# Performance work log

Hardware: AMD Instinct MI355X
Metric: run time of the kernel (lower is better)

## Reference

```python
import jax, jax.numpy as jnp
import numpy as np

B, T, C, NH = 8, 512, 512, 8
HD = C // NH

def _layernorm(x, g, b, eps=1e-5):
    mu = jnp.mean(x, axis=-1, keepdims=True)
    var = jnp.var(x, axis=-1, keepdims=True)
    return (x - mu) * jax.lax.rsqrt(var + eps) * g + b

def setup_inputs() -> dict:
    key = jax.random.key(0)
    ks = jax.random.split(key, 5)
    return {
        "x": jax.random.normal(ks[0], (B, T, C), jnp.float32),
        "w_attn": jax.random.normal(ks[1], (3 * C, C), jnp.float32) * (1.0 / np.sqrt(C)),
        "b_attn": jnp.zeros((3 * C,), jnp.float32),
        "w_proj": jax.random.normal(ks[2], (C, C), jnp.float32) * (1.0 / np.sqrt(C)),
        "b_proj": jnp.zeros((C,), jnp.float32),
        "q_gamma": jnp.ones((C,), jnp.float32),
        "q_beta": jnp.zeros((C,), jnp.float32),
        "k_gamma": jnp.ones((C,), jnp.float32),
        "k_beta": jnp.zeros((C,), jnp.float32),
        "rel_emb": jax.random.normal(ks[3], (T, C), jnp.float32) * 0.02,
    }

def reference(x, w_attn, b_attn, w_proj, b_proj, q_gamma, q_beta, k_gamma, k_beta, rel_emb):
    b, t, c = x.shape
    # QKV projection (torch Linear: x @ W.T + b)
    qkv = x @ w_attn.T + b_attn                       # [B,T,3C]
    q, k, v = jnp.split(qkv, 3, axis=-1)
    # per-stream LayerNorm over full embedding dim (q_ln/k_ln = LayerNorm(n_embd))
    q = _layernorm(q, q_gamma, q_beta)
    k = _layernorm(k, k_gamma, k_beta)
    # split heads -> [B,NH,T,HD]
    q = q.reshape(b, t, NH, HD).transpose(0, 2, 1, 3)
    k = k.reshape(b, t, NH, HD).transpose(0, 2, 1, 3)
    v = v.reshape(b, t, NH, HD).transpose(0, 2, 1, 3)
    # relative-position bias: gather rel_emb[|i-j|] -> [T,T,NH,HD]
    idx = jnp.abs(jnp.arange(t)[None, :] - jnp.arange(t)[:, None])  # [T,T] int
    rel = rel_emb[idx].reshape(t, t, NH, HD)
    rel_bias = jnp.einsum("bhqd,qkhd->bhqk", q, rel)  # [B,NH,T,T]
    scale = 1.0 / np.sqrt(HD)
    scores = (jnp.einsum("bhqd,bhkd->bhqk", q, k) + rel_bias) * scale
    causal = jnp.tril(jnp.ones((t, t), bool))
    scores = jnp.where(causal[None, None], scores, jnp.finfo(scores.dtype).min)
    att = jax.nn.softmax(scores, axis=-1)
    y = jnp.einsum("bhqk,bhkd->bhqd", att, v)         # [B,NH,T,HD]
    y = y.transpose(0, 2, 1, 3).reshape(b, t, c)
    return y @ w_proj.T + b_proj
```

## Files before the change

kernel.cpp:

```cpp
#include <hip/hip_runtime.h>
#include <hip/hip_bf16.h>
#include <cstddef>

#define BB 8
#define TT 512
#define CC 512
#define NHH 8
#define HDD 64

typedef __attribute__((ext_vector_type(8))) short short8;
typedef __attribute__((ext_vector_type(4))) float f32x4;

__device__ __forceinline__ unsigned short f2bf(float f) {
    unsigned u = __float_as_uint(f);
    u += 0x7FFFu + ((u >> 16) & 1u);
    return (unsigned short)(u >> 16);
}
__device__ __forceinline__ float bf2f(unsigned short h) {
    return __uint_as_float(((unsigned)h) << 16);
}

__global__ __launch_bounds__(256) void cvt_all_k(
    const float* __restrict__ x, const float* __restrict__ wa,
    const float* __restrict__ wp, const float* __restrict__ rel,
    unsigned short* __restrict__ Xb, unsigned short* __restrict__ Wqb,
    unsigned short* __restrict__ Wpb, unsigned short* __restrict__ Relb)
{
    const int bidx = blockIdx.x;
    const float* in;
    unsigned short* out;
    int base;
    if (bidx < 2048)      { in = x;   out = Xb;   base = bidx; }
    else if (bidx < 2816) { in = wa;  out = Wqb;  base = bidx - 2048; }
    else if (bidx < 3072) { in = wp;  out = Wpb;  base = bidx - 2816; }
    else                  { in = rel; out = Relb; base = bidx - 3072; }
    const int i = base * 1024 + threadIdx.x * 4;
    const float4 v = *(const float4*)(in + i);
    unsigned short tmp[4] = {f2bf(v.x), f2bf(v.y), f2bf(v.z), f2bf(v.w)};
    *(uint2*)(out + i) = *(const uint2*)tmp;
}

__global__ __launch_bounds__(256, 2) void gemm_qkv_mfma(
    const unsigned short* __restrict__ Xb, const unsigned short* __restrict__ Wb,
    const float* __restrict__ bias, unsigned short* __restrict__ qkbuf,
    unsigned short* __restrict__ VT)
{
    __shared__ __align__(16) unsigned short lds[128 * 136];

    const int tid = threadIdx.x;
    const int w = tid >> 6, lane = tid & 63;
    const int c = lane & 15, quad = lane >> 4;
    const int wm = w >> 1, wn = w & 1;
    const int bm = blockIdx.y * 128, bn = blockIdx.x * 128;

    const unsigned short* pp[8];
#pragma unroll
    for (int l = 0; l < 8; ++l) {
        const int ci = w * 8 + l;
        if (ci < 16) {
            const int m16 = ci >> 1, kk = ci & 1;
            pp[l] = Xb + (size_t)(bm + m16 * 16 + c) * 512 + kk * 32 + quad * 8;
        } else {
            const int cb = ci - 16, n16 = cb >> 1, kk = cb & 1;
            pp[l] = Wb + (size_t)(bn + n16 * 16 + c) * 512 + kk * 32 + quad * 8;
        }
    }

    f32x4 acc[4][4];
#pragma unroll
    for (int i = 0; i < 4; ++i)
#pragma unroll
        for (int j = 0; j < 4; ++j) acc[i][j] = (f32x4){0.f, 0.f, 0.f, 0.f};

    short8 pre[8];
#pragma unroll
    for (int l = 0; l < 8; ++l) pre[l] = *(const short8*)pp[l];

    for (int k0 = 0; k0 < 512; k0 += 64) {
        __syncthreads();
#pragma unroll
        for (int l = 0; l < 8; ++l)
            *(short8*)&lds[(w * 8 + l) * 512 + lane * 8] = pre[l];
        __syncthreads();
        if (k0 + 64 < 512) {
#pragma unroll
            for (int l = 0; l < 8; ++l)
                pre[l] = *(const short8*)(pp[l] + k0 + 64);
        }
#pragma unroll
        for (int kk = 0; kk < 2; ++kk) {
            short8 af[4], bfr[4];
#pragma unroll
            for (int i = 0; i < 4; ++i)
                af[i] = *(const short8*)&lds[((wm * 4 + i) * 2 + kk) * 512 + lane * 8];
#pragma unroll
            for (int j = 0; j < 4; ++j)
                bfr[j] = *(const short8*)&lds[(16 + (wn * 4 + j) * 2 + kk) * 512 + lane * 8];
#pragma unroll
            for (int i = 0; i < 4; ++i)
#pragma unroll
                for (int j = 0; j < 4; ++j)
                    acc[i][j] = __builtin_amdgcn_mfma_f32_16x16x32_bf16(
                        af[i], bfr[j], acc[i][j], 0, 0, 0);
        }
    }

    float bj[4];
#pragma unroll
    for (int j = 0; j < 4; ++j) bj[j] = bias[bn + wn * 64 + j * 16 + c];

    if (bn < 1024) {
#pragma unroll
        for (int i = 0; i < 4; ++i)
#pragma unroll
            for (int j = 0; j < 4; ++j) {
                const int n = bn + wn * 64 + j * 16 + c;
#pragma unroll
                for (int r = 0; r < 4; ++r) {
                    const int m = bm + wm * 64 + i * 16 + quad * 4 + r;
                    qkbuf[(size_t)m * 1024 + n] = f2bf(acc[i][j][r] + bj[j]);
                }
            }
    } else {
        __syncthreads();
#pragma unroll
        for (int i = 0; i < 4; ++i)
#pragma unroll
            for (int j = 0; j < 4; ++j) {
                const int col = wn * 64 + j * 16 + c;
                const int row0 = wm * 64 + i * 16 + quad * 4;
                unsigned short t4[4];
#pragma unroll
                for (int r = 0; r < 4; ++r) t4[r] = f2bf(acc[i][j][r] + bj[j]);
                *(uint2*)&lds[col * 136 + row0] = *(const uint2*)t4;
            }
        __syncthreads();
        const int bi = bm >> 9, tb = bm & 511;
        const int hd0 = bn - 1024;
#pragma unroll
        for (int l = 0; l < 8; ++l) {
            const int idx = l * 256 + tid;
            const int col = idx >> 4, grp = idx & 15;
            const short8 v = *(const short8*)&lds[col * 136 + grp * 8];
            const int hd = hd0 + col, h = hd >> 6, d = hd & 63;
            *(short8*)(VT + ((size_t)(bi * NHH + h) * HDD + d) * TT + tb + grp * 8) = v;
        }
    }
}

__global__ __launch_bounds__(256) void ln_k(
    const unsigned short* __restrict__ qkbuf,
    const float* __restrict__ qg, const float* __restrict__ qb,
    const float* __restrict__ kg, const float* __restrict__ kb,
    unsigned short* __restrict__ Qh, unsigned short* __restrict__ Kh)
{
    const int wv = threadIdx.x >> 6, lane = threadIdx.x & 63;
    const int row = blockIdx.x * 4 + wv;
    const int bi = row >> 9, t = row & 511;
    const unsigned short* base = qkbuf + (size_t)row * 1024;

#pragma unroll
    for (int s = 0; s < 2; ++s) {
        const short8 v8 = *(const short8*)(base + s * 512 + lane * 8);
        float vf[8];
#pragma unroll
        for (int i = 0; i < 8; ++i) vf[i] = bf2f(((const unsigned short*)&v8)[i]);
        float sum = 0.f, sq = 0.f;
#pragma unroll
        for (int i = 0; i < 8; ++i) { sum += vf[i]; sq += vf[i] * vf[i]; }
#pragma unroll
        for (int off = 1; off < 64; off <<= 1) {
            sum += __shfl_xor(sum, off);
            sq += __shfl_xor(sq, off);
        }
        const float mu = sum * (1.f / 512.f);
        const float var = sq * (1.f / 512.f) - mu * mu;
        const float rsg = rsqrtf(var + 1e-5f);
        const float* gam = (s ? kg : qg) + lane * 8;
        const float* bet = (s ? kb : qb) + lane * 8;
        const float4 g0 = *(const float4*)gam, g1 = *(const float4*)(gam + 4);
        const float4 b0 = *(const float4*)bet, b1 = *(const float4*)(bet + 4);
        const float gv[8] = {g0.x, g0.y, g0.z, g0.w, g1.x, g1.y, g1.z, g1.w};
        const float bv[8] = {b0.x, b0.y, b0.z, b0.w, b1.x, b1.y, b1.z, b1.w};
        unsigned short o8[8];
#pragma unroll
        for (int i = 0; i < 8; ++i)
            o8[i] = f2bf((vf[i] - mu) * rsg * gv[i] + bv[i]);
        unsigned short* outp = s ? Kh : Qh;
        *(short8*)(outp + ((size_t)(bi * NHH + (lane >> 3)) * TT + t) * HDD
                   + (lane & 7) * 8) = *(const short8*)o8;
    }
}

#define RD_BODY(nr_)                                                            \
    {                                                                           \
        const short8 br0 = *(const short8*)&Rels[((nr_) * 2 + 0) * 512 + lane * 8]; \
        const short8 br1 = *(const short8*)&Rels[((nr_) * 2 + 1) * 512 + lane * 8]; \
        f32x4 a2 = (f32x4){0.f, 0.f, 0.f, 0.f};                                 \
        a2 = __builtin_amdgcn_mfma_f32_16x16x32_bf16(aq0, br0, a2, 0, 0, 0);    \
        a2 = __builtin_amdgcn_mfma_f32_16x16x32_bf16(aq1, br1, a2, 0, 0, 0);    \
        const int colw = (mbase + (nr_) * 16 + c) & 127;                        \
        _Pragma("unroll")                                                       \
        for (int r = 0; r < 4; ++r)                                             \
            RDs[w][(quad * 4 + r) * 132 + colw] = f2bf(a2[r]);                  \
    }

__global__ __launch_bounds__(256, 2) void attn_k(
    const unsigned short* __restrict__ Qh, const unsigned short* __restrict__ Kh,
    const unsigned short* __restrict__ VT, const unsigned short* __restrict__ Relb,
    unsigned short* __restrict__ Yb)
{
    __shared__ __align__(16) unsigned short Qs[8 * 512];
    __shared__ __align__(16) unsigned short Ks[8 * 512];
    __shared__ __align__(16) unsigned short Vs[8 * 512];
    __shared__ __align__(16) unsigned short Rels[16 * 512];
    __shared__ __align__(16) unsigned short Ps[4][16 * 72];
    __shared__ __align__(16) unsigned short RDs[4][16 * 132];

    const int tid = threadIdx.x;
    const int w = tid >> 6;
    const int lane = tid & 63;
    const int c = lane & 15;
    const int quad = lane >> 4;

    const int bid = blockIdx.x;
    const int bit0 = bid & 1, bit8 = (bid >> 8) & 1;
    const int s_ = bit0 ^ bit8;
    const int q0 = (bid >> 1) & 7;
    const int qt = s_ ? 7 - q0 : q0;
    const int h = (bid >> 4) & 7;
    const int b = ((bid >> 7) & 1) | (bit8 << 1) | (bit0 << 2);
    const int i0 = qt * 64;

    const unsigned short* Qbase = Qh + (size_t)(b * NHH + h) * TT * HDD;
    const unsigned short* Kbase = Kh + (size_t)(b * NHH + h) * TT * HDD;
    const unsigned short* Vbase = VT + (size_t)(b * NHH + h) * HDD * TT;
    const unsigned short* Rbase = Relb + h * HDD;

#pragma unroll
    for (int kk = 0; kk < 2; ++kk) {
        const unsigned short* gp =
            Qbase + (size_t)(i0 + w * 16 + c) * HDD + kk * 32 + quad * 8;
        *(short8*)&Qs[(w * 2 + kk) * 512 + lane * 8] = *(const short8*)gp;
    }

    f32x4 oacc[4];
    float m_i[4], l_i[4];
#pragma unroll
    for (int r = 0; r < 4; ++r) { m_i[r] = -1e30f; l_i[r] = 0.f; }
#pragma unroll
    for (int nd = 0; nd < 4; ++nd) oacc[nd] = (f32x4){0.f, 0.f, 0.f, 0.f};

    short8 aq0, aq1;

    for (int jt = 0; jt <= qt; ++jt) {
        const int j0 = jt * 64;
#pragma unroll
        for (int kk = 0; kk < 2; ++kk) {
            const unsigned short* gp =
                Kbase + (size_t)(j0 + w * 16 + c) * HDD + kk * 32 + quad * 8;
            *(short8*)&Ks[(w * 2 + kk) * 512 + lane * 8] = *(const short8*)gp;
        }
#pragma unroll
        for (int js = 0; js < 2; ++js) {
            const unsigned short* gp =
                Vbase + (size_t)(w * 16 + c) * TT + j0 + js * 32 + quad * 8;
            *(short8*)&Vs[(w * 2 + js) * 512 + lane * 8] = *(const short8*)gp;
        }
        const int mbase = i0 - j0 - 63;
        if (jt == 0) {
#pragma unroll
            for (int sb = 0; sb < 2; ++sb) {
#pragma unroll
                for (int kk = 0; kk < 2; ++kk) {
                    const int n16 = w * 2 + sb;
                    int mrow = mbase + n16 * 16 + c;
                    mrow = mrow < 0 ? 0 : (mrow > 511 ? 511 : mrow);
                    *(short8*)&Rels[(n16 * 2 + kk) * 512 + lane * 8] =
                        *(const short8*)(Rbase + (size_t)mrow * CC + kk * 32 + quad * 8);
                }
            }
        } else {
#pragma unroll
            for (int kk = 0; kk < 2; ++kk) {
                int mrow = mbase + w * 16 + c;
                mrow = mrow < 0 ? 0 : (mrow > 511 ? 511 : mrow);
                *(short8*)&Rels[(w * 2 + kk) * 512 + lane * 8] =
                    *(const short8*)(Rbase + (size_t)mrow * CC + kk * 32 + quad * 8);
            }
        }
        __syncthreads();

        if (jt == 0) {
            aq0 = *(const short8*)&Qs[(w * 2 + 0) * 512 + lane * 8];
            aq1 = *(const short8*)&Qs[(w * 2 + 1) * 512 + lane * 8];
        }

        f32x4 sAcc[4];
#pragma unroll
        for (int ns = 0; ns < 4; ++ns) {
            const short8 bk0 = *(const short8*)&Ks[(ns * 2 + 0) * 512 + lane * 8];
            const short8 bk1 = *(const short8*)&Ks[(ns * 2 + 1) * 512 + lane * 8];
            f32x4 a2 = (f32x4){0.f, 0.f, 0.f, 0.f};
            a2 = __builtin_amdgcn_mfma_f32_16x16x32_bf16(aq0, bk0, a2, 0, 0, 0);
            a2 = __builtin_amdgcn_mfma_f32_16x16x32_bf16(aq1, bk1, a2, 0, 0, 0);
            sAcc[ns] = a2;
        }
        if (jt == 0) {
#pragma unroll
            for (int nr = 0; nr < 8; ++nr) RD_BODY(nr)
        } else {
#pragma unroll
            for (int nr = 0; nr < 4; ++nr) RD_BODY(nr)
        }

        const int dbase = i0 - j0;
        float sc[4][4];
#pragma unroll
        for (int ns = 0; ns < 4; ++ns) {
#pragma unroll
            for (int r = 0; r < 4; ++r) {
                const int r16 = quad * 4 + r;
                const int jc = ns * 16 + c;
                const int dp = (dbase + w * 16 + r16 - jc) & 127;
                const float rdv = bf2f(RDs[w][r16 * 132 + dp]);
                const float v = (sAcc[ns][r] + rdv) * 0.125f;
                sc[ns][r] = (j0 + jc > i0 + w * 16 + r16) ? -1e30f : v;
            }
        }
        float alpha[4];
#pragma unroll
        for (int r = 0; r < 4; ++r) {
            float m = fmaxf(fmaxf(sc[0][r], sc[1][r]), fmaxf(sc[2][r], sc[3][r]));
#pragma unroll
            for (int off = 1; off < 16; off <<= 1) m = fmaxf(m, __shfl_xor(m, off));
            const float mn = fmaxf(m_i[r], m);
            alpha[r] = __expf(m_i[r] - mn);
            m_i[r] = mn;
        }
        float rs[4] = {0.f, 0.f, 0.f, 0.f};
#pragma unroll
        for (int ns = 0; ns < 4; ++ns) {
#pragma unroll
            for (int r = 0; r < 4; ++r) {
                const float p = __expf(sc[ns][r] - m_i[r]);
                rs[r] += p;
                Ps[w][(quad * 4 + r) * 72 + ns * 16 + c] = f2bf(p);
            }
        }
#pragma unroll
        for (int r = 0; r < 4; ++r) {
#pragma unroll
            for (int off = 1; off < 16; off <<= 1) rs[r] += __shfl_xor(rs[r], off);
            l_i[r] = l_i[r] * alpha[r] + rs[r];
        }
#pragma unroll
        for (int nd = 0; nd < 4; ++nd)
#pragma unroll
            for (int r = 0; r < 4; ++r) oacc[nd][r] *= alpha[r];

        const short8 ap0 = *(const short8*)&Ps[w][c * 72 + 0 * 32 + quad * 8];
        const short8 ap1 = *(const short8*)&Ps[w][c * 72 + 1 * 32 + quad * 8];
#pragma unroll
        for (int nd = 0; nd < 4; ++nd) {
            const short8 bv0 = *(const short8*)&Vs[(nd * 2 + 0) * 512 + lane * 8];
            const short8 bv1 = *(const short8*)&Vs[(nd * 2 + 1) * 512 + lane * 8];
            oacc[nd] = __builtin_amdgcn_mfma_f32_16x16x32_bf16(ap0, bv0, oacc[nd], 0, 0, 0);
            oacc[nd] = __builtin_amdgcn_mfma_f32_16x16x32_bf16(ap1, bv1, oacc[nd], 0, 0, 0);
        }
        __syncthreads();
    }

#pragma unroll
    for (int r = 0; r < 4; ++r) {
        const float inv = 1.f / l_i[r];
        const int trow = i0 + w * 16 + quad * 4 + r;
        unsigned short* yb = Yb + ((size_t)b * TT + trow) * CC + h * HDD;
#pragma unroll
        for (int nd = 0; nd < 4; ++nd)
            yb[nd * 16 + c] = f2bf(oacc[nd][r] * inv);
    }
}

__global__ __launch_bounds__(256, 2) void gemm_proj_mfma(
    const unsigned short* __restrict__ Yb, const unsigned short* __restrict__ Wp,
    const float* __restrict__ bias, float* __restrict__ out)
{
    __shared__ __align__(16) unsigned short lds[24 * 512];

    const int tid = threadIdx.x;
    const int w = tid >> 6, lane = tid & 63;
    const int c = lane & 15, quad = lane >> 4;
    const int wm = w >> 1, wn = w & 1;
    const int bm = blockIdx.y * 64, bn = blockIdx.x * 128;

    const unsigned short* pp[6];
#pragma unroll
    for (int l = 0; l < 6; ++l) {
        const int ci = w * 6 + l;
        if (ci < 8) {
            const int m16 = ci >> 1, kk = ci & 1;
            pp[l] = Yb + (size_t)(bm + m16 * 16 + c) * 512 + kk * 32 + quad * 8;
        } else {
            const int cb = ci - 8, n16 = cb >> 1, kk = cb & 1;
            pp[l] = Wp + (size_t)(bn + n16 * 16 + c) * 512 + kk * 32 + quad * 8;
        }
    }

    f32x4 acc[2][4];
#pragma unroll
    for (int i = 0; i < 2; ++i)
#pragma unroll
        for (int j = 0; j < 4; ++j) acc[i][j] = (f32x4){0.f, 0.f, 0.f, 0.f};

    short8 pre[6];
#pragma unroll
    for (int l = 0; l < 6; ++l) pre[l] = *(const short8*)pp[l];

    for (int k0 = 0; k0 < 512; k0 += 64) {
        __syncthreads();
#pragma unroll
        for (int l = 0; l < 6; ++l)
            *(short8*)&lds[(w * 6 + l) * 512 + lane * 8] = pre[l];
        __syncthreads();
        if (k0 + 64 < 512) {
#pragma unroll
            for (int l = 0; l < 6; ++l)
                pre[l] = *(const short8*)(pp[l] + k0 + 64);
        }
#pragma unroll
        for (int kk = 0; kk < 2; ++kk) {
            short8 af[2], bfr[4];
#pragma unroll
            for (int i = 0; i < 2; ++i)
                af[i] = *(const short8*)&lds[((wm * 2 + i) * 2 + kk) * 512 + lane * 8];
#pragma unroll
            for (int j = 0; j < 4; ++j)
                bfr[j] = *(const short8*)&lds[(8 + (wn * 4 + j) * 2 + kk) * 512 + lane * 8];
#pragma unroll
            for (int i = 0; i < 2; ++i)
#pragma unroll
                for (int j = 0; j < 4; ++j)
                    acc[i][j] = __builtin_amdgcn_mfma_f32_16x16x32_bf16(
                        af[i], bfr[j], acc[i][j], 0, 0, 0);
        }
    }

#pragma unroll
    for (int j = 0; j < 4; ++j) {
        const int n = bn + wn * 64 + j * 16 + c;
        const float bj = bias[n];
#pragma unroll
        for (int i = 0; i < 2; ++i)
#pragma unroll
            for (int r = 0; r < 4; ++r) {
                const int m = bm + wm * 32 + i * 16 + quad * 4 + r;
                out[(size_t)m * 512 + n] = acc[i][j][r] + bj;
            }
    }
}

extern "C" void kernel_launch(void* const* d_in, const int* in_sizes, int n_in,
                              void* d_out, int out_size, void* d_ws, size_t ws_size,
                              hipStream_t stream)
{
    const float* x      = (const float*)d_in[0];
    const float* w_attn = (const float*)d_in[1];
    const float* b_attn = (const float*)d_in[2];
    const float* w_proj = (const float*)d_in[3];
    const float* b_proj = (const float*)d_in[4];
    const float* q_g    = (const float*)d_in[5];
    const float* q_b    = (const float*)d_in[6];
    const float* k_g    = (const float*)d_in[7];
    const float* k_b    = (const float*)d_in[8];
    const float* rel    = (const float*)d_in[9];
    float* out = (float*)d_out;

    unsigned short* qkbuf = (unsigned short*)d_ws;
    unsigned short* Qh   = qkbuf + (size_t)4096 * 1024;
    unsigned short* Kh   = Qh + (size_t)4096 * 512;
    unsigned short* VT   = Kh + (size_t)4096 * 512;
    unsigned short* Relb = VT + (size_t)4096 * 512;
    unsigned short* Xb   = Relb + (size_t)512 * 512;
    unsigned short* Wqb  = Xb + (size_t)4096 * 512;
    unsigned short* Wpb  = Wqb + (size_t)1536 * 512;
    unsigned short* Yb   = qkbuf;

    cvt_all_k<<<3328, 256, 0, stream>>>(x, w_attn, w_proj, rel, Xb, Wqb, Wpb, Relb);
    gemm_qkv_mfma<<<dim3(12, 32), 256, 0, stream>>>(Xb, Wqb, b_attn, qkbuf, VT);
    ln_k<<<1024, 256, 0, stream>>>(qkbuf, q_g, q_b, k_g, k_b, Qh, Kh);
    attn_k<<<512, 256, 0, stream>>>(Qh, Kh, VT, Relb, Yb);
    gemm_proj_mfma<<<dim3(4, 64), 256, 0, stream>>>(Yb, Wpb, b_proj, out);
}
```

Baseline: 141.6 us.

## Load attention MFMA operands directly from global memory, dropping shared staging

The attention kernel no longer stages Q, K, V and relative-embedding tiles through shared memory. Each wave loads its MFMA fragments straight from global memory into registers, which removes the per-iteration block barriers and the LDS round trips. The first-tile extra rel-bias blocks are computed once before the loop. In exchange, each wave redundantly fetches the full K/V tiles (four times the global/L2 traffic per block) and uses more registers, which may lower occupancy.

```diff
diff --git a/kernel.cpp b/kernel.cpp
--- a/kernel.cpp
+++ b/kernel.cpp
@@ -192,14 +192,17 @@
     }
 }
 
-#define RD_BODY(nr_)                                                            \
+#define RD_DIRECT(nr_, mb_)                                                     \
     {                                                                           \
-        const short8 br0 = *(const short8*)&Rels[((nr_) * 2 + 0) * 512 + lane * 8]; \
-        const short8 br1 = *(const short8*)&Rels[((nr_) * 2 + 1) * 512 + lane * 8]; \
+        int mrow = (mb_) + (nr_) * 16 + c;                                      \
+        mrow = mrow < 0 ? 0 : (mrow > 511 ? 511 : mrow);                        \
+        const unsigned short* gp = Rbase + (size_t)mrow * CC + quad * 8;        \
+        const short8 br0 = *(const short8*)gp;                                  \
+        const short8 br1 = *(const short8*)(gp + 32);                           \
         f32x4 a2 = (f32x4){0.f, 0.f, 0.f, 0.f};                                 \
         a2 = __builtin_amdgcn_mfma_f32_16x16x32_bf16(aq0, br0, a2, 0, 0, 0);    \
         a2 = __builtin_amdgcn_mfma_f32_16x16x32_bf16(aq1, br1, a2, 0, 0, 0);    \
-        const int colw = (mbase + (nr_) * 16 + c) & 127;                        \
+        const int colw = ((mb_) + (nr_) * 16 + c) & 127;                        \
         _Pragma("unroll")                                                       \
         for (int r = 0; r < 4; ++r)                                             \
             RDs[w][(quad * 4 + r) * 132 + colw] = f2bf(a2[r]);                  \
@@ -210,10 +213,6 @@
     const unsigned short* __restrict__ VT, const unsigned short* __restrict__ Relb,
     unsigned short* __restrict__ Yb)
 {
-    __shared__ __align__(16) unsigned short Qs[8 * 512];
-    __shared__ __align__(16) unsigned short Ks[8 * 512];
-    __shared__ __align__(16) unsigned short Vs[8 * 512];
-    __shared__ __align__(16) unsigned short Rels[16 * 512];
     __shared__ __align__(16) unsigned short Ps[4][16 * 72];
     __shared__ __align__(16) unsigned short RDs[4][16 * 132];
 
@@ -237,12 +236,9 @@
     const unsigned short* Vbase = VT + (size_t)(b * NHH + h) * HDD * TT;
     const unsigned short* Rbase = Relb + h * HDD;
 
-#pragma unroll
-    for (int kk = 0; kk < 2; ++kk) {
-        const unsigned short* gp =
-            Qbase + (size_t)(i0 + w * 16 + c) * HDD + kk * 32 + quad * 8;
-        *(short8*)&Qs[(w * 2 + kk) * 512 + lane * 8] = *(const short8*)gp;
-    }
+    const unsigned short* qp = Qbase + (size_t)(i0 + w * 16 + c) * HDD + quad * 8;
+    const short8 aq0 = *(const short8*)qp;
+    const short8 aq1 = *(const short8*)(qp + 32);
 
     f32x4 oacc[4];
     float m_i[4], l_i[4];
@@ -251,67 +247,42 @@
 #pragma unroll
     for (int nd = 0; nd < 4; ++nd) oacc[nd] = (f32x4){0.f, 0.f, 0.f, 0.f};
 
-    short8 aq0, aq1;
+    {
+        const int mb0 = i0 - 63;
+#pragma unroll
+        for (int nr = 4; nr < 8; ++nr) RD_DIRECT(nr, mb0)
+    }
 
     for (int jt = 0; jt <= qt; ++jt) {
         const int j0 = jt * 64;
-#pragma unroll
-        for (int kk = 0; kk < 2; ++kk) {
-            const unsigned short* gp =
-                Kbase + (size_t)(j0 + w * 16 + c) * HDD + kk * 32 + quad * 8;
-            *(short8*)&Ks[(w * 2 + kk) * 512 + lane * 8] = *(const short8*)gp;
-        }
-#pragma unroll
-        for (int js = 0; js < 2; ++js) {
-            const unsigned short* gp =
-                Vbase + (size_t)(w * 16 + c) * TT + j0 + js * 32 + quad * 8;
-            *(short8*)&Vs[(w * 2 + js) * 512 + lane * 8] = *(const short8*)gp;
-        }
         const int mbase = i0 - j0 - 63;
-        if (jt == 0) {
-#pragma unroll
-            for (int sb = 0; sb < 2; ++sb) {
-#pragma unroll
-                for (int kk = 0; kk < 2; ++kk) {
-                    const int n16 = w * 2 + sb;
-                    int mrow = mbase + n16 * 16 + c;
-                    mrow = mrow < 0 ? 0 : (mrow > 511 ? 511 : mrow);
-                    *(short8*)&Rels[(n16 * 2 + kk) * 512 + lane * 8] =
-                        *(const short8*)(Rbase + (size_t)mrow * CC + kk * 32 + quad * 8);
-                }
-            }
-        } else {
-#pragma unroll
-            for (int kk = 0; kk < 2; ++kk) {
-                int mrow = mbase + w * 16 + c;
-                mrow = mrow < 0 ? 0 : (mrow > 511 ? 511 : mrow);
-                *(short8*)&Rels[(w * 2 + kk) * 512 + lane * 8] =
-                    *(const short8*)(Rbase + (size_t)mrow * CC + kk * 32 + quad * 8);
-            }
-        }
-        __syncthreads();
-
-        if (jt == 0) {
-            aq0 = *(const short8*)&Qs[(w * 2 + 0) * 512 + lane * 8];
-            aq1 = *(const short8*)&Qs[(w * 2 + 1) * 512 + lane * 8];
-        }
+
+        short8 bk0[4], bk1[4], bv0[4], bv1[4];
+#pragma unroll
+        for (int ns = 0; ns < 4; ++ns) {
+            const unsigned short* kp =
+                Kbase + (size_t)(j0 + ns * 16 + c) * HDD + quad * 8;
+            bk0[ns] = *(const short8*)kp;
+            bk1[ns] = *(const short8*)(kp + 32);
+        }
+#pragma unroll
+        for (int nd = 0; nd < 4; ++nd) {
+            const unsigned short* vp =
+                Vbase + (size_t)(nd * 16 + c) * TT + j0 + quad * 8;
+            bv0[nd] = *(const short8*)vp;
+            bv1[nd] = *(const short8*)(vp + 32);
+        }
+
+#pragma unroll
+        for (int nr = 0; nr < 4; ++nr) RD_DIRECT(nr, mbase)
 
         f32x4 sAcc[4];
 #pragma unroll
         for (int ns = 0; ns < 4; ++ns) {
-            const short8 bk0 = *(const short8*)&Ks[(ns * 2 + 0) * 512 + lane * 8];
-            const short8 bk1 = *(const short8*)&Ks[(ns * 2 + 1) * 512 + lane * 8];
             f32x4 a2 = (f32x4){0.f, 0.f, 0.f, 0.f};
-            a2 = __builtin_amdgcn_mfma_f32_16x16x32_bf16(aq0, bk0, a2, 0, 0, 0);
-            a2 = __builtin_amdgcn_mfma_f32_16x16x32_bf16(aq1, bk1, a2, 0, 0, 0);
+            a2 = __builtin_amdgcn_mfma_f32_16x16x32_bf16(aq0, bk0[ns], a2, 0, 0, 0);
+            a2 = __builtin_amdgcn_mfma_f32_16x16x32_bf16(aq1, bk1[ns], a2, 0, 0, 0);
             sAcc[ns] = a2;
-        }
-        if (jt == 0) {
-#pragma unroll
-            for (int nr = 0; nr < 8; ++nr) RD_BODY(nr)
-        } else {
-#pragma unroll
-            for (int nr = 0; nr < 4; ++nr) RD_BODY(nr)
         }
 
         const int dbase = i0 - j0;
@@ -363,12 +334,9 @@
         const short8 ap1 = *(const short8*)&Ps[w][c * 72 + 1 * 32 + quad * 8];
 #pragma unroll
         for (int nd = 0; nd < 4; ++nd) {
-            const short8 bv0 = *(const short8*)&Vs[(nd * 2 + 0) * 512 + lane * 8];
-            const short8 bv1 = *(const short8*)&Vs[(nd * 2 + 1) * 512 + lane * 8];
-            oacc[nd] = __builtin_amdgcn_mfma_f32_16x16x32_bf16(ap0, bv0, oacc[nd], 0, 0, 0);
-            oacc[nd] = __builtin_amdgcn_mfma_f32_16x16x32_bf16(ap1, bv1, oacc[nd], 0, 0, 0);
-        }
-        __syncthreads();
+            oacc[nd] = __builtin_amdgcn_mfma_f32_16x16x32_bf16(ap0, bv0[nd], oacc[nd], 0, 0, 0);
+            oacc[nd] = __builtin_amdgcn_mfma_f32_16x16x32_bf16(ap1, bv1[nd], oacc[nd], 0, 0, 0);
+        }
     }
 
 #pragma unroll
```

Result: no change. 142.9 us (+0.9%).

## Fuse LayerNorm into QKV GEMM epilogue stats and attention tile loads

Applied to the files above, without the earlier changes.

Removes the standalone LayerNorm kernel. The QKV GEMM epilogue now reduces per-row sum and sum-of-squares and atomically adds them into a stats buffer, which a new zero kernel clears first. Attention normalizes Q and K on the fly while loading tiles from the raw qkbuf. This saves a launch and a full read/write pass over Q and K, but K normalization is recomputed per query tile, adds float atomics and per-element gamma/beta loads, and computes stats from fp32 values instead of bf16-rounded ones.

```diff
diff --git a/kernel.cpp b/kernel.cpp
--- a/kernel.cpp
+++ b/kernel.cpp
@@ -18,6 +18,12 @@
 }
 __device__ __forceinline__ float bf2f(unsigned short h) {
     return __uint_as_float(((unsigned)h) << 16);
+}
+
+__global__ __launch_bounds__(256) void zero_stats_k(float* __restrict__ Stats)
+{
+    const int i = (blockIdx.x * 256 + threadIdx.x) * 4;
+    *(float4*)(Stats + i) = make_float4(0.f, 0.f, 0.f, 0.f);
 }
 
 __global__ __launch_bounds__(256) void cvt_all_k(
@@ -43,7 +49,7 @@
 __global__ __launch_bounds__(256, 2) void gemm_qkv_mfma(
     const unsigned short* __restrict__ Xb, const unsigned short* __restrict__ Wb,
     const float* __restrict__ bias, unsigned short* __restrict__ qkbuf,
-    unsigned short* __restrict__ VT)
+    unsigned short* __restrict__ VT, float* __restrict__ Stats)
 {
     __shared__ __align__(16) unsigned short lds[128 * 136];
 
@@ -110,6 +116,11 @@
     for (int j = 0; j < 4; ++j) bj[j] = bias[bn + wn * 64 + j * 16 + c];
 
     if (bn < 1024) {
+        float sv[4][4], sq2[4][4];
+#pragma unroll
+        for (int i = 0; i < 4; ++i)
+#pragma unroll
+            for (int r = 0; r < 4; ++r) { sv[i][r] = 0.f; sq2[i][r] = 0.f; }
 #pragma unroll
         for (int i = 0; i < 4; ++i)
 #pragma unroll
@@ -117,10 +128,27 @@
                 const int n = bn + wn * 64 + j * 16 + c;
 #pragma unroll
                 for (int r = 0; r < 4; ++r) {
+                    const float v = acc[i][j][r] + bj[j];
+                    sv[i][r] += v;
+                    sq2[i][r] += v * v;
                     const int m = bm + wm * 64 + i * 16 + quad * 4 + r;
-                    qkbuf[(size_t)m * 1024 + n] = f2bf(acc[i][j][r] + bj[j]);
+                    qkbuf[(size_t)m * 1024 + n] = f2bf(v);
                 }
             }
+#pragma unroll
+        for (int off = 1; off < 16; off <<= 1)
+#pragma unroll
+            for (int i = 0; i < 4; ++i)
+#pragma unroll
+                for (int r = 0; r < 4; ++r) {
+                    sv[i][r] += __shfl_xor(sv[i][r], off);
+                    sq2[i][r] += __shfl_xor(sq2[i][r], off);
+                }
+        const int ii = c >> 2, rr = c & 3;
+        const int row = bm + wm * 64 + ii * 16 + quad * 4 + rr;
+        const int strm = bn >> 9;
+        atomicAdd(&Stats[row * 4 + strm * 2 + 0], sv[ii][rr]);
+        atomicAdd(&Stats[row * 4 + strm * 2 + 1], sq2[ii][rr]);
     } else {
         __syncthreads();
 #pragma unroll
@@ -145,50 +173,6 @@
             const int hd = hd0 + col, h = hd >> 6, d = hd & 63;
             *(short8*)(VT + ((size_t)(bi * NHH + h) * HDD + d) * TT + tb + grp * 8) = v;
         }
-    }
-}
-
-__global__ __launch_bounds__(256) void ln_k(
-    const unsigned short* __restrict__ qkbuf,
-    const float* __restrict__ qg, const float* __restrict__ qb,
-    const float* __restrict__ kg, const float* __restrict__ kb,
-    unsigned short* __restrict__ Qh, unsigned short* __restrict__ Kh)
-{
-    const int wv = threadIdx.x >> 6, lane = threadIdx.x & 63;
-    const int row = blockIdx.x * 4 + wv;
-    const int bi = row >> 9, t = row & 511;
-    const unsigned short* base = qkbuf + (size_t)row * 1024;
-
-#pragma unroll
-    for (int s = 0; s < 2; ++s) {
-        const short8 v8 = *(const short8*)(base + s * 512 + lane * 8);
-        float vf[8];
-#pragma unroll
-        for (int i = 0; i < 8; ++i) vf[i] = bf2f(((const unsigned short*)&v8)[i]);
-        float sum = 0.f, sq = 0.f;
-#pragma unroll
-        for (int i = 0; i < 8; ++i) { sum += vf[i]; sq += vf[i] * vf[i]; }
-#pragma unroll
-        for (int off = 1; off < 64; off <<= 1) {
-            sum += __shfl_xor(sum, off);
-            sq += __shfl_xor(sq, off);
-        }
-        const float mu = sum * (1.f / 512.f);
-        const float var = sq * (1.f / 512.f) - mu * mu;
-        const float rsg = rsqrtf(var + 1e-5f);
-        const float* gam = (s ? kg : qg) + lane * 8;
-        const float* bet = (s ? kb : qb) + lane * 8;
-        const float4 g0 = *(const float4*)gam, g1 = *(const float4*)(gam + 4);
-        const float4 b0 = *(const float4*)bet, b1 = *(const float4*)(bet + 4);
-        const float gv[8] = {g0.x, g0.y, g0.z, g0.w, g1.x, g1.y, g1.z, g1.w};
-        const float bv[8] = {b0.x, b0.y, b0.z, b0.w, b1.x, b1.y, b1.z, b1.w};
-        unsigned short o8[8];
-#pragma unroll
-        for (int i = 0; i < 8; ++i)
-            o8[i] = f2bf((vf[i] - mu) * rsg * gv[i] + bv[i]);
-        unsigned short* outp = s ? Kh : Qh;
-        *(short8*)(outp + ((size_t)(bi * NHH + (lane >> 3)) * TT + t) * HDD
-                   + (lane & 7) * 8) = *(const short8*)o8;
     }
 }
 
@@ -206,8 +190,10 @@
     }
 
 __global__ __launch_bounds__(256, 2) void attn_k(
-    const unsigned short* __restrict__ Qh, const unsigned short* __restrict__ Kh,
-    const unsigned short* __restrict__ VT, const unsigned short* __restrict__ Relb,
+    const unsigned short* __restrict__ qkbuf, const unsigned short* __restrict__ VT,
+    const unsigned short* __restrict__ Relb, const float* __restrict__ Stats,
+    const float* __restrict__ qg, const float* __restrict__ qb,
+    const float* __restrict__ kg, const float* __restrict__ kb,
     unsigned short* __restrict__ Yb)
 {
     __shared__ __align__(16) unsigned short Qs[8 * 512];
@@ -232,16 +218,39 @@
     const int b = ((bid >> 7) & 1) | (bit8 << 1) | (bit0 << 2);
     const int i0 = qt * 64;
 
-    const unsigned short* Qbase = Qh + (size_t)(b * NHH + h) * TT * HDD;
-    const unsigned short* Kbase = Kh + (size_t)(b * NHH + h) * TT * HDD;
     const unsigned short* Vbase = VT + (size_t)(b * NHH + h) * HDD * TT;
     const unsigned short* Rbase = Relb + h * HDD;
 
-#pragma unroll
-    for (int kk = 0; kk < 2; ++kk) {
-        const unsigned short* gp =
-            Qbase + (size_t)(i0 + w * 16 + c) * HDD + kk * 32 + quad * 8;
-        *(short8*)&Qs[(w * 2 + kk) * 512 + lane * 8] = *(const short8*)gp;
+    float kgv[2][8], kbv[2][8];
+#pragma unroll
+    for (int kk = 0; kk < 2; ++kk)
+#pragma unroll
+        for (int e = 0; e < 8; ++e) {
+            const int chan = h * 64 + kk * 32 + quad * 8 + e;
+            kgv[kk][e] = kg[chan];
+            kbv[kk][e] = kb[chan];
+        }
+
+    {
+        const int trow = i0 + w * 16 + c;
+        const float2 st = *(const float2*)&Stats[(b * 512 + trow) * 4 + 0];
+        const float mu = st.x * (1.f / 512.f);
+        const float var = st.y * (1.f / 512.f) - mu * mu;
+        const float rsg = rsqrtf(var + 1e-5f);
+#pragma unroll
+        for (int kk = 0; kk < 2; ++kk) {
+            const unsigned short* gp = qkbuf + (size_t)(b * 512 + trow) * 1024
+                                       + h * 64 + kk * 32 + quad * 8;
+            const short8 raw = *(const short8*)gp;
+            unsigned short o8[8];
+#pragma unroll
+            for (int e = 0; e < 8; ++e) {
+                const int chan = h * 64 + kk * 32 + quad * 8 + e;
+                o8[e] = f2bf((bf2f(((const unsigned short*)&raw)[e]) - mu) * rsg
+                             * qg[chan] + qb[chan]);
+            }
+            *(short8*)&Qs[(w * 2 + kk) * 512 + lane * 8] = *(const short8*)o8;
+        }
     }
 
     f32x4 oacc[4];
@@ -255,11 +264,24 @@
 
     for (int jt = 0; jt <= qt; ++jt) {
         const int j0 = jt * 64;
-#pragma unroll
-        for (int kk = 0; kk < 2; ++kk) {
-            const unsigned short* gp =
-                Kbase + (size_t)(j0 + w * 16 + c) * HDD + kk * 32 + quad * 8;
-            *(short8*)&Ks[(w * 2 + kk) * 512 + lane * 8] = *(const short8*)gp;
+        {
+            const int krow = j0 + w * 16 + c;
+            const float2 st = *(const float2*)&Stats[(b * 512 + krow) * 4 + 2];
+            const float mu = st.x * (1.f / 512.f);
+            const float var = st.y * (1.f / 512.f) - mu * mu;
+            const float rsg = rsqrtf(var + 1e-5f);
+#pragma unroll
+            for (int kk = 0; kk < 2; ++kk) {
+                const unsigned short* gp = qkbuf + (size_t)(b * 512 + krow) * 1024
+                                           + 512 + h * 64 + kk * 32 + quad * 8;
+                const short8 raw = *(const short8*)gp;
+                unsigned short o8[8];
+#pragma unroll
+                for (int e = 0; e < 8; ++e)
+                    o8[e] = f2bf((bf2f(((const unsigned short*)&raw)[e]) - mu) * rsg
+                                 * kgv[kk][e] + kbv[kk][e]);
+                *(short8*)&Ks[(w * 2 + kk) * 512 + lane * 8] = *(const short8*)o8;
+            }
         }
 #pragma unroll
         for (int js = 0; js < 2; ++js) {
@@ -477,18 +499,17 @@
     float* out = (float*)d_out;
 
     unsigned short* qkbuf = (unsigned short*)d_ws;
-    unsigned short* Qh   = qkbuf + (size_t)4096 * 1024;
-    unsigned short* Kh   = Qh + (size_t)4096 * 512;
-    unsigned short* VT   = Kh + (size_t)4096 * 512;
+    unsigned short* Yb   = qkbuf + (size_t)4096 * 1024;
+    unsigned short* VT   = Yb + (size_t)4096 * 512;
     unsigned short* Relb = VT + (size_t)4096 * 512;
     unsigned short* Xb   = Relb + (size_t)512 * 512;
     unsigned short* Wqb  = Xb + (size_t)4096 * 512;
     unsigned short* Wpb  = Wqb + (size_t)1536 * 512;
-    unsigned short* Yb   = qkbuf;
-
+    float* Stats = (float*)(Wpb + (size_t)512 * 512);
+
+    zero_stats_k<<<16, 256, 0, stream>>>(Stats);
     cvt_all_k<<<3328, 256, 0, stream>>>(x, w_attn, w_proj, rel, Xb, Wqb, Wpb, Relb);
-    gemm_qkv_mfma<<<dim3(12, 32), 256, 0, stream>>>(Xb, Wqb, b_attn, qkbuf, VT);
-    ln_k<<<1024, 256, 0, stream>>>(qkbuf, q_g, q_b, k_g, k_b, Qh, Kh);
-    attn_k<<<512, 256, 0, stream>>>(Qh, Kh, VT, Relb, Yb);
+    gemm_qkv_mfma<<<dim3(12, 32), 256, 0, stream>>>(Xb, Wqb, b_attn, qkbuf, VT, Stats);
+    attn_k<<<512, 256, 0, stream>>>(qkbuf, VT, Relb, Stats, q_g, q_b, k_g, k_b, Yb);
     gemm_proj_mfma<<<dim3(4, 64), 256, 0, stream>>>(Yb, Wpb, b_proj, out);
 }
```

After: 148.3 us. +4.8%, slower.
